# Kernel tuning notes

Measured on AMD Instinct MI355X. Metric: run time of the kernel, lower is better.

Reference implementation:

```python
import jax, jax.numpy as jnp
import numpy as np

N_NODES = 50000
N_EDGES = 800000
HID = 256
HEADS = 4
HEAD_C = HID // HEADS  # 64
IN_CH = 16
OUT_CH = 4
NEG_SLOPE = 0.2  # PyG GATConv default LeakyReLU slope
LN_EPS = 1e-5


def setup_inputs() -> dict:
    key = jax.random.key(0)
    ks = jax.random.split(key, 12)
    s = 0.05
    return {
        "x": jax.random.normal(ks[0], (N_NODES, IN_CH), dtype=jnp.float32),
        "edge_index": jax.random.randint(ks[1], (2, N_EDGES), 0, N_NODES, dtype=jnp.int64),
        "w_in": jax.random.normal(ks[2], (IN_CH, HID), dtype=jnp.float32) * s,
        "b_in": jnp.zeros((HID,), dtype=jnp.float32),
        "w_gat": jax.random.normal(ks[3], (4, HID, HID), dtype=jnp.float32) * s,
        "att_src": jax.random.normal(ks[4], (4, HEADS, HEAD_C), dtype=jnp.float32) * s,
        "att_dst": jax.random.normal(ks[5], (4, HEADS, HEAD_C), dtype=jnp.float32) * s,
        "b_gat": jnp.zeros((4, HID), dtype=jnp.float32),
        "ln_scale": jnp.ones((4, HID), dtype=jnp.float32),
        "ln_bias": jnp.zeros((4, HID), dtype=jnp.float32),
        "w_out": jax.random.normal(ks[6], (HID, OUT_CH), dtype=jnp.float32) * s,
        "b_out": jnp.zeros((OUT_CH,), dtype=jnp.float32),
    }


def _gat_layer(x, src, dst, W, a_src, a_dst, bias, g, beta):
    """One GATConv(concat, heads=4) + LayerNorm + ELU. x:[N,HID]."""
    n = x.shape[0]
    h = (x @ W).reshape(n, HEADS, HEAD_C)                 # [N,H,C]
    a_s = jnp.einsum("nhc,hc->nh", h, a_src)              # [N,H]
    a_d = jnp.einsum("nhc,hc->nh", h, a_dst)              # [N,H]
    logits = jax.nn.leaky_relu(a_s[src] + a_d[dst], NEG_SLOPE)  # [E,H]
    # segment softmax over destination neighborhoods (self-loops ensure non-empty)
    m = jax.ops.segment_max(logits, dst, num_segments=n)
    e = jnp.exp(logits - m[dst])
    denom = jax.ops.segment_sum(e, dst, num_segments=n)
    alpha = e / (denom[dst] + 1e-16)                      # [E,H]
    msg = alpha[:, :, None] * h[src]                      # [E,H,C]
    out = jax.ops.segment_sum(msg, dst, num_segments=n).reshape(n, HID) + bias
    mu = out.mean(-1, keepdims=True)
    var = out.var(-1, keepdims=True)
    out = (out - mu) * jax.lax.rsqrt(var + LN_EPS) * g + beta
    return jax.nn.elu(out)


def reference(x, edge_index, w_in, b_in, w_gat, att_src, att_dst, b_gat,
              ln_scale, ln_bias, w_out, b_out):
    n = x.shape[0]
    # PyG GATConv adds self-loops by default
    loops = jnp.arange(n, dtype=edge_index.dtype)
    ei = jnp.concatenate([edge_index, jnp.stack([loops, loops])], axis=1)
    src, dst = ei[0], ei[1]

    x = x @ w_in + b_in                                   # input_proj
    h = x
    for l in (0, 1):
        h = _gat_layer(h, src, dst, w_gat[l], att_src[l], att_dst[l],
                       b_gat[l], ln_scale[l], ln_bias[l])
    x = x + h
    h = x
    for l in (2, 3):
        h = _gat_layer(h, src, dst, w_gat[l], att_src[l], att_dst[l],
                       b_gat[l], ln_scale[l], ln_bias[l])
    x = x + h
    return x @ w_out + b_out
```

## Files before the change

kernel.cpp:

```cpp
#include <hip/hip_runtime.h>
#include <math.h>

#define NN 50000
#define E0 800000
#define ET 850000
#define HID 256
#define INCH 16
#define MAXDEG 64

#define NB_P1   416
#define EPB     2048
#define NBUCK   196

#define NB_WT   256
#define NB_IP   6250
#define NB_PREP (NB_P1 + NB_WT + NB_IP)

#define NB_G    784
#define NB_G0   (NBUCK + NB_G)

typedef _Float16 h8 __attribute__((ext_vector_type(8)));
typedef _Float16 h4 __attribute__((ext_vector_type(4)));
typedef float f32x4 __attribute__((ext_vector_type(4)));

__device__ __forceinline__ void load_lds16(const void* g, void* l) {
    __builtin_amdgcn_global_load_lds(
        (const __attribute__((address_space(1))) unsigned int*)g,
        (__attribute__((address_space(3))) unsigned int*)l, 16, 0, 0);
}

__global__ __launch_bounds__(256) void prep_kernel(
    const float* __restrict__ w_gat, _Float16* __restrict__ WT,
    const float* __restrict__ x, const float* __restrict__ w_in,
    const float* __restrict__ b_in, _Float16* __restrict__ Ph,
    const int* __restrict__ ei, unsigned int* __restrict__ pairs,
    int* __restrict__ cnt_g, int* __restrict__ off_g) {
    __shared__ unsigned int hist[256], pref[256], cur2[256];
    int b = blockIdx.x, t = threadIdx.x;
    if (b < NB_P1) {
        hist[t] = 0;
        __syncthreads();
        unsigned int pk[8];
        int base = b * EPB + t;
#pragma unroll
        for (int k = 0; k < 8; ++k) {
            int e = base + k * 256;
            pk[k] = 0xFFFFFFFFu;
            if (e < ET) {
                int s, d;
                if (e < E0) { s = ei[e]; d = ei[E0 + e]; }
                else        { s = d = e - E0; }
                pk[k] = ((unsigned int)d << 16) | (unsigned int)s;
                atomicAdd(&hist[d >> 8], 1u);
            }
        }
        __syncthreads();
        unsigned int h = hist[t];
        pref[t] = h;
        __syncthreads();
#pragma unroll
        for (int o = 1; o < 256; o <<= 1) {
            unsigned int v = (t >= o) ? pref[t - o] : 0u;
            __syncthreads();
            pref[t] += v;
            __syncthreads();
        }
        unsigned int ex = pref[t] - h;
        cur2[t] = ex;
        if (t < NBUCK) {
            cnt_g[b * NBUCK + t] = (int)h;
            off_g[b * NBUCK + t] = (int)ex;
        }
        __syncthreads();
#pragma unroll
        for (int k = 0; k < 8; ++k) {
            if (pk[k] != 0xFFFFFFFFu) {
                unsigned int g = pk[k] >> 24;
                unsigned int pos = atomicAdd(&cur2[g], 1u);
                pairs[b * EPB + pos] = pk[k];
            }
        }
    } else if (b < NB_P1 + NB_WT) {
        int k = b - NB_P1;
#pragma unroll
        for (int l = 0; l < 4; ++l) {
            float v = w_gat[((size_t)l * 256 + k) * 256 + t];
            WT[((size_t)l * 256 + t) * 256 + k] = (_Float16)v;
        }
    } else {
        int ipb = b - NB_P1 - NB_WT;
        int sub = t >> 5, l32 = t & 31;
        int n = ipb * 8 + sub;
        int c0 = l32 * 8;
        const float* xr = x + n * INCH;
        float a[8];
#pragma unroll
        for (int k = 0; k < 8; k += 4) {
            float4 bb = *(const float4*)(b_in + c0 + k);
            a[k] = bb.x; a[k + 1] = bb.y; a[k + 2] = bb.z; a[k + 3] = bb.w;
        }
#pragma unroll
        for (int k = 0; k < INCH; ++k) {
            float xv = xr[k];
            const float4 w0 = *(const float4*)(w_in + k * 256 + c0);
            const float4 w1 = *(const float4*)(w_in + k * 256 + c0 + 4);
            a[0] += xv * w0.x; a[1] += xv * w0.y; a[2] += xv * w0.z; a[3] += xv * w0.w;
            a[4] += xv * w1.x; a[5] += xv * w1.y; a[6] += xv * w1.z; a[7] += xv * w1.w;
        }
        h8 o;
#pragma unroll
        for (int k = 0; k < 8; ++k) o[k] = (_Float16)a[k];
        *(h8*)(Ph + (size_t)n * 256 + c0) = o;
    }
}

__device__ __forceinline__ void gemm_tile(
    int rb, int cb,
    const _Float16* __restrict__ A, const _Float16* __restrict__ BT,
    _Float16* __restrict__ H, const float* __restrict__ att_s,
    const float* __restrict__ att_d, float* __restrict__ AS, float* __restrict__ AD,
    _Float16* As, _Float16* Bs) {
    int t = threadIdx.x;
    int wv = t >> 6, lane = t & 63;
    int wr = (wv >> 1) * 64, wc = (wv & 1) * 64;
    int lm = lane & 15, lq = lane >> 4;
    f32x4 acc[4][4] = {};

    int rch = lane >> 2;
    int q = lane & 3;

    auto stage = [&](int k0, int buf) {
#pragma unroll
        for (int c = 0; c < 2; ++c) {
            int r = wv * 32 + c * 16 + rch;
            int g = q ^ (r & 3);
            int ra = rb + r; if (ra >= NN) ra = NN - 1;
            load_lds16(A + (size_t)ra * 256 + k0 + g * 8,
                       (char*)As + buf * 8192 + wv * 2048 + c * 1024);
            load_lds16(BT + (size_t)(cb + r) * 256 + k0 + g * 8,
                       (char*)Bs + buf * 8192 + wv * 2048 + c * 1024);
        }
    };

    stage(0, 0);
    __syncthreads();
    int cur = 0;
    for (int k0 = 0; k0 < 256; k0 += 32) {
        if (k0 + 32 < 256) stage(k0 + 32, cur ^ 1);
        h8 af[4], bfr[4];
#pragma unroll
        for (int i = 0; i < 4; ++i) {
            int row = wr + i * 16 + lm;
            af[i] = *(const h8*)((const char*)As + cur * 8192 + row * 64 + ((lq ^ (row & 3)) * 16));
        }
#pragma unroll
        for (int j = 0; j < 4; ++j) {
            int row = wc + j * 16 + lm;
            bfr[j] = *(const h8*)((const char*)Bs + cur * 8192 + row * 64 + ((lq ^ (row & 3)) * 16));
        }
#pragma unroll
        for (int i = 0; i < 4; ++i)
#pragma unroll
            for (int j = 0; j < 4; ++j)
                acc[i][j] = __builtin_amdgcn_mfma_f32_16x16x32_f16(af[i], bfr[j], acc[i][j], 0, 0, 0);
        __syncthreads();
        cur ^= 1;
    }

    int head = (cb + wc) >> 6;
    float sa[4], sd[4];
#pragma unroll
    for (int j = 0; j < 4; ++j) {
        sa[j] = att_s[head * 64 + j * 16 + lm];
        sd[j] = att_d[head * 64 + j * 16 + lm];
    }
#pragma unroll
    for (int i = 0; i < 4; ++i)
#pragma unroll
        for (int rr = 0; rr < 4; ++rr) {
            float vs = acc[i][0][rr] * sa[0] + acc[i][1][rr] * sa[1]
                     + acc[i][2][rr] * sa[2] + acc[i][3][rr] * sa[3];
            float vd = acc[i][0][rr] * sd[0] + acc[i][1][rr] * sd[1]
                     + acc[i][2][rr] * sd[2] + acc[i][3][rr] * sd[3];
#pragma unroll
            for (int o = 1; o <= 8; o <<= 1) {
                vs += __shfl_xor(vs, o, 64);
                vd += __shfl_xor(vd, o, 64);
            }
            int row = rb + wr + i * 16 + lq * 4 + rr;
            if (lm == 0 && row < NN) {
                AS[row * 4 + head] = vs;
                AD[row * 4 + head] = vd;
            }
        }

#pragma unroll
    for (int i = 0; i < 4; ++i)
#pragma unroll
        for (int j = 0; j < 4; ++j) {
            int col = cb + wc + j * 16 + lm;
#pragma unroll
            for (int rr = 0; rr < 4; ++rr) {
                int row = rb + wr + i * 16 + lq * 4 + rr;
                if (row < NN) H[(size_t)row * 256 + col] = (_Float16)acc[i][j][rr];
            }
        }
}

__device__ __forceinline__ bool gemm_map(int b, int& rb, int& cb) {
    int r = (b >> 4) * 8 + (b & 7);
    int h = (b >> 3) & 1;
    if (r >= 391) return false;
    rb = r * 128; cb = h * 128;
    return true;
}

__global__ __launch_bounds__(256) void gemm_fused_kernel(
    const _Float16* __restrict__ A, const _Float16* __restrict__ BT,
    _Float16* __restrict__ H, const float* __restrict__ att_s,
    const float* __restrict__ att_d, float* __restrict__ AS, float* __restrict__ AD) {
    __shared__ _Float16 As[2 * 128 * 32];
    __shared__ _Float16 Bs[2 * 128 * 32];
    int rb, cb;
    if (!gemm_map(blockIdx.x, rb, cb)) return;
    gemm_tile(rb, cb, A, BT, H, att_s, att_d, AS, AD, As, Bs);
}

__global__ __launch_bounds__(256) void gemm0_p2_kernel(
    const _Float16* __restrict__ A, const _Float16* __restrict__ BT,
    _Float16* __restrict__ H, const float* __restrict__ att_s,
    const float* __restrict__ att_d, float* __restrict__ AS, float* __restrict__ AD,
    const unsigned int* __restrict__ pairs, const int* __restrict__ cnt_g,
    const int* __restrict__ off_g, int* __restrict__ cursor,
    unsigned short* __restrict__ csr_pad) {
    __shared__ _Float16 As[2 * 128 * 32];
    __shared__ _Float16 Bs[2 * 128 * 32];
    int b = blockIdx.x;
    if (b < NBUCK) {
        int g = b, t = threadIdx.x;
        unsigned int* curs = (unsigned int*)As;
        curs[t] = 0;
        __syncthreads();
        for (int sb = t; sb < NB_P1; sb += 256) {
            int c = cnt_g[sb * NBUCK + g];
            int o = off_g[sb * NBUCK + g];
            const unsigned int* p = pairs + sb * EPB + o;
            for (int i = 0; i < c; ++i) {
                unsigned int pk = p[i];
                int d = (int)(pk >> 16);
                unsigned int pos = atomicAdd(&curs[d & 255], 1u);
                if (pos < MAXDEG)
                    csr_pad[((size_t)d << 6) + pos] = (unsigned short)(pk & 0xFFFFu);
            }
        }
        __syncthreads();
        int n = (g << 8) + t;
        if (n < NN) cursor[n] = (int)curs[t];
        return;
    }
    int rb, cb;
    if (!gemm_map(b - NBUCK, rb, cb)) return;
    gemm_tile(rb, cb, A, BT, H, att_s, att_d, AS, AD, As, Bs);
}

__global__ __launch_bounds__(256) void agg_kernel(
    const _Float16* __restrict__ H, const float4* __restrict__ AS,
    const float4* __restrict__ AD,
    const int* __restrict__ cnt, const unsigned short* __restrict__ csr_pad,
    const float* __restrict__ bias, const float* __restrict__ g, const float* __restrict__ beta,
    const _Float16* __restrict__ res, _Float16* __restrict__ outh,
    const float* __restrict__ wout, const float* __restrict__ bout,
    float* __restrict__ out) {
    __shared__ float eLs[4][256];
    __shared__ int   sLs[4][64];
    int t = threadIdx.x;
    int wv = t >> 6, lane = t & 63;
    int n = blockIdx.x * 4 + wv;
    int head = lane >> 4;
    int c0 = lane * 4;
    float* eL = eLs[wv];
    int*   sL = sLs[wv];

    int deg = cnt[n];
    if (deg > MAXDEG) deg = MAXDEG;
    float4 adv = AD[n];

    float4 e4 = make_float4(0.f, 0.f, 0.f, 0.f);
    int sv = 0;
    if (lane < deg) {
        sv = csr_pad[(n << 6) + lane];
        float4 as = AS[sv];
        float v0 = as.x + adv.x; v0 = (v0 >= 0.f) ? v0 : 0.2f * v0;
        float v1 = as.y + adv.y; v1 = (v1 >= 0.f) ? v1 : 0.2f * v1;
        float v2 = as.z + adv.z; v2 = (v2 >= 0.f) ? v2 : 0.2f * v2;
        float v3 = as.w + adv.w; v3 = (v3 >= 0.f) ? v3 : 0.2f * v3;
        e4 = make_float4(__expf(v0), __expf(v1), __expf(v2), __expf(v3));
    }
    sL[lane] = sv;
    *(float4*)(eL + c0) = e4;

    float acc0 = 0.f, acc1 = 0.f, acc2 = 0.f, acc3 = 0.f, acc_e = 0.f;
#pragma unroll 8
    for (int i = 0; i < deg; ++i) {
        float e = eL[i * 4 + head];
        int s = sL[i];
        h4 hv = *(const h4*)(H + (size_t)s * 256 + c0);
        acc_e += e;
        acc0 += e * (float)hv[0];
        acc1 += e * (float)hv[1];
        acc2 += e * (float)hv[2];
        acc3 += e * (float)hv[3];
    }
    float dinv = 1.f / (acc_e + 1e-16f);

    float4 bb = *(const float4*)(bias + c0);
    float val0 = acc0 * dinv + bb.x;
    float val1 = acc1 * dinv + bb.y;
    float val2 = acc2 * dinv + bb.z;
    float val3 = acc3 * dinv + bb.w;

    float s1 = val0 + val1 + val2 + val3;
    float s2 = val0 * val0 + val1 * val1 + val2 * val2 + val3 * val3;
#pragma unroll
    for (int o = 32; o >= 1; o >>= 1) {
        s1 += __shfl_xor(s1, o, 64);
        s2 += __shfl_xor(s2, o, 64);
    }
    float mu = s1 * (1.f / 256.f);
    float var = s2 * (1.f / 256.f) - mu * mu;
    float rs = rsqrtf(var + 1e-5f);

    float4 g4 = *(const float4*)(g + c0);
    float4 b4 = *(const float4*)(beta + c0);
    float y0 = (val0 - mu) * rs * g4.x + b4.x;
    float y1 = (val1 - mu) * rs * g4.y + b4.y;
    float y2 = (val2 - mu) * rs * g4.z + b4.z;
    float y3 = (val3 - mu) * rs * g4.w + b4.w;
    y0 = (y0 > 0.f) ? y0 : (__expf(y0) - 1.f);
    y1 = (y1 > 0.f) ? y1 : (__expf(y1) - 1.f);
    y2 = (y2 > 0.f) ? y2 : (__expf(y2) - 1.f);
    y3 = (y3 > 0.f) ? y3 : (__expf(y3) - 1.f);
    if (res) {
        h4 r0 = *(const h4*)(res + (size_t)n * 256 + c0);
        y0 += (float)r0[0]; y1 += (float)r0[1]; y2 += (float)r0[2]; y3 += (float)r0[3];
    }
    if (wout) {
        float4 w0 = *(const float4*)(wout + (size_t)(c0 + 0) * 4);
        float4 w1 = *(const float4*)(wout + (size_t)(c0 + 1) * 4);
        float4 w2 = *(const float4*)(wout + (size_t)(c0 + 2) * 4);
        float4 w3 = *(const float4*)(wout + (size_t)(c0 + 3) * 4);
        float o0 = y0 * w0.x + y1 * w1.x + y2 * w2.x + y3 * w3.x;
        float o1 = y0 * w0.y + y1 * w1.y + y2 * w2.y + y3 * w3.y;
        float o2 = y0 * w0.z + y1 * w1.z + y2 * w2.z + y3 * w3.z;
        float o3 = y0 * w0.w + y1 * w1.w + y2 * w2.w + y3 * w3.w;
#pragma unroll
        for (int o = 32; o >= 1; o >>= 1) {
            o0 += __shfl_xor(o0, o, 64);
            o1 += __shfl_xor(o1, o, 64);
            o2 += __shfl_xor(o2, o, 64);
            o3 += __shfl_xor(o3, o, 64);
        }
        if (lane == 0) {
            float4 ov = make_float4(o0 + bout[0], o1 + bout[1], o2 + bout[2], o3 + bout[3]);
            *(float4*)(out + (size_t)n * 4) = ov;
        }
    } else {
        h4 o0;
        o0[0] = (_Float16)y0; o0[1] = (_Float16)y1;
        o0[2] = (_Float16)y2; o0[3] = (_Float16)y3;
        *(h4*)(outh + (size_t)n * 256 + c0) = o0;
    }
}

extern "C" void kernel_launch(void* const* d_in, const int* in_sizes, int n_in,
                              void* d_out, int out_size, void* d_ws, size_t ws_size,
                              hipStream_t stream) {
    const float* x       = (const float*)d_in[0];
    const int*   ei      = (const int*)  d_in[1];
    const float* w_in    = (const float*)d_in[2];
    const float* b_in    = (const float*)d_in[3];
    const float* w_gat   = (const float*)d_in[4];
    const float* att_src = (const float*)d_in[5];
    const float* att_dst = (const float*)d_in[6];
    const float* b_gat   = (const float*)d_in[7];
    const float* ln_g    = (const float*)d_in[8];
    const float* ln_b    = (const float*)d_in[9];
    const float* w_out   = (const float*)d_in[10];
    const float* b_out   = (const float*)d_in[11];
    float* out = (float*)d_out;

    char* ws = (char*)d_ws;
    size_t off = 0;
    auto alloc = [&](size_t bytes) {
        void* p = ws + off;
        off += (bytes + 255) & ~(size_t)255;
        return p;
    };
    _Float16*       Ph      = (_Float16*)alloc((size_t)NN * HID * 2);
    _Float16*       Ch      = (_Float16*)alloc((size_t)NN * HID * 2);
    _Float16*       Gh      = (_Float16*)alloc((size_t)NN * HID * 2);
    _Float16*       H       = (_Float16*)alloc((size_t)NN * HID * 2);
    _Float16*       WT      = (_Float16*)alloc((size_t)4 * HID * HID * 2);
    float*          ASAD    = (float*)alloc((size_t)NN * 8 * 4);
    int*            cursor  = (int*)alloc((size_t)NN * 4);
    unsigned short* csr_pad = (unsigned short*)alloc((size_t)NN * MAXDEG * 2);
    unsigned int*   pairs   = (unsigned int*)alloc((size_t)NB_P1 * EPB * 4);
    int*            cnt_g   = (int*)alloc((size_t)NB_P1 * NBUCK * 4);
    int*            off_g   = (int*)alloc((size_t)NB_P1 * NBUCK * 4);

    float* AS = ASAD;
    float* AD = ASAD + (size_t)NN * 4;

    const int NB_AGG = NN / 4;

    prep_kernel<<<NB_PREP, 256, 0, stream>>>(w_gat, WT, x, w_in, b_in, Ph,
                                             ei, pairs, cnt_g, off_g);

    gemm0_p2_kernel<<<NB_G0, 256, 0, stream>>>(
        Ph, WT, H, att_src, att_dst, AS, AD, pairs, cnt_g, off_g, cursor, csr_pad);
    agg_kernel<<<NB_AGG, 256, 0, stream>>>(
        H, (const float4*)AS, (const float4*)AD, cursor, csr_pad,
        b_gat, ln_g, ln_b, nullptr, Gh, nullptr, nullptr, nullptr);

    auto run_layer = [&](const _Float16* inh, int l, const _Float16* res, _Float16* outh,
                         const float* wo, const float* bo) {
        gemm_fused_kernel<<<NB_G, 256, 0, stream>>>(
            inh, WT + (size_t)l * HID * HID, H,
            att_src + l * 256, att_dst + l * 256, AS, AD);
        agg_kernel<<<NB_AGG, 256, 0, stream>>>(
            H, (const float4*)AS, (const float4*)AD, cursor, csr_pad,
            b_gat + l * 256, ln_g + l * 256, ln_b + l * 256, res, outh, wo, bo,
            wo ? out : nullptr);
    };

    run_layer(Gh, 1, Ph,      Ch, nullptr, nullptr);
    run_layer(Ch, 2, nullptr, Gh, nullptr, nullptr);
    run_layer(Gh, 3, Ch,      Ph, w_out,   b_out);
}
```

Measured before the change: 506.5 us.

## Split aggregation into per-slice gather kernels with slice-major H and separate LayerNorm

The GEMM now writes H in a slice-major layout of 8 column slices of 32 halves per node. A new slice aggregation kernel gathers neighbours one slice at a time, with block index mod 8 picking the slice. The intent is that each XCD gathers from a ~3.2MB slice that can stay resident in its L2, instead of scattering 512B row reads over the full 25.6MB H. Softmax normalisation moves into the slice kernel, and LayerNorm, ELU, residual and output projection move to a separate kernel that reads an fp16 intermediate. This adds an extra round trip to global memory and an extra launch per layer.

```diff
diff --git a/kernel.cpp b/kernel.cpp
--- a/kernel.cpp
+++ b/kernel.cpp
@@ -18,6 +18,11 @@
 
 #define NB_G    784
 #define NB_G0   (NBUCK + NB_G)
+
+#define NPW_S   8
+#define NB_SL   (8 * ((NN + 4 * NPW_S - 1) / (4 * NPW_S)))
+#define NPW_L   4
+#define NB_LN   (NN / (4 * NPW_L))
 
 typedef _Float16 h8 __attribute__((ext_vector_type(8)));
 typedef _Float16 h4 __attribute__((ext_vector_type(4)));
@@ -199,10 +204,11 @@
 #pragma unroll
         for (int j = 0; j < 4; ++j) {
             int col = cb + wc + j * 16 + lm;
+            _Float16* Hc = H + (size_t)(col >> 5) * NN * 32 + (col & 31);
 #pragma unroll
             for (int rr = 0; rr < 4; ++rr) {
                 int row = rb + wr + i * 16 + lq * 4 + rr;
-                if (row < NN) H[(size_t)row * 256 + col] = (_Float16)acc[i][j][rr];
+                if (row < NN) Hc[(size_t)row * 32] = (_Float16)acc[i][j][rr];
             }
         }
 }
@@ -263,112 +269,142 @@
     gemm_tile(rb, cb, A, BT, H, att_s, att_d, AS, AD, As, Bs);
 }
 
-__global__ __launch_bounds__(256) void agg_kernel(
-    const _Float16* __restrict__ H, const float4* __restrict__ AS,
-    const float4* __restrict__ AD,
+__global__ __launch_bounds__(256) void slice_agg_kernel(
+    const _Float16* __restrict__ H,
+    const float* __restrict__ AS,
+    const float* __restrict__ AD,
     const int* __restrict__ cnt, const unsigned short* __restrict__ csr_pad,
+    _Float16* __restrict__ tmp) {
+    __shared__ float alS[4][80];
+    __shared__ int   slS[4][80];
+    int t = threadIdx.x;
+    int wv = t >> 6, lane = t & 63;
+    int b = blockIdx.x;
+    int s = b & 7;
+    int h = s >> 1;
+    int grp = b >> 3;
+    const _Float16* Hs = H + (size_t)s * NN * 32;
+    float* al = alS[wv];
+    int*   sl = slS[wv];
+    int eg = lane >> 3;
+    int cc = (lane & 7) * 4;
+
+    for (int k = 0; k < NPW_S; ++k) {
+        int n = (grp * 4 + wv) * NPW_S + k;
+        if (n >= NN) break;
+        int deg = cnt[n];
+        if (deg > MAXDEG) deg = MAXDEG;
+        float e_i = 0.f;
+        int sv = 0;
+        if (lane < deg) {
+            sv = csr_pad[(n << 6) + lane];
+            float v = AS[sv * 4 + h] + AD[n * 4 + h];
+            v = (v >= 0.f) ? v : 0.2f * v;
+            e_i = __expf(v);
+        }
+        float den = e_i;
+#pragma unroll
+        for (int o = 1; o <= 32; o <<= 1) den += __shfl_xor(den, o, 64);
+        float alpha = e_i / den;
+        al[lane] = alpha;
+        sl[lane] = sv;
+        if (lane < 16) { al[64 + lane] = 0.f; sl[64 + lane] = 0; }
+        float a0 = 0.f, a1 = 0.f, a2 = 0.f, a3 = 0.f;
+        for (int i = 0; i < deg; i += 8) {
+            int e = i + eg;
+            float a = al[e];
+            int src = sl[e];
+            h4 hv = *(const h4*)(Hs + (size_t)src * 32 + cc);
+            a0 += a * (float)hv[0];
+            a1 += a * (float)hv[1];
+            a2 += a * (float)hv[2];
+            a3 += a * (float)hv[3];
+        }
+#pragma unroll
+        for (int o = 8; o <= 32; o <<= 1) {
+            a0 += __shfl_xor(a0, o, 64);
+            a1 += __shfl_xor(a1, o, 64);
+            a2 += __shfl_xor(a2, o, 64);
+            a3 += __shfl_xor(a3, o, 64);
+        }
+        if (lane < 8) {
+            h4 ov;
+            ov[0] = (_Float16)a0; ov[1] = (_Float16)a1;
+            ov[2] = (_Float16)a2; ov[3] = (_Float16)a3;
+            *(h4*)(tmp + (size_t)n * 256 + s * 32 + lane * 4) = ov;
+        }
+    }
+}
+
+__global__ __launch_bounds__(256) void ln_kernel(
+    const _Float16* __restrict__ tmp,
     const float* __restrict__ bias, const float* __restrict__ g, const float* __restrict__ beta,
     const _Float16* __restrict__ res, _Float16* __restrict__ outh,
     const float* __restrict__ wout, const float* __restrict__ bout,
     float* __restrict__ out) {
-    __shared__ float eLs[4][256];
-    __shared__ int   sLs[4][64];
     int t = threadIdx.x;
     int wv = t >> 6, lane = t & 63;
-    int n = blockIdx.x * 4 + wv;
-    int head = lane >> 4;
     int c0 = lane * 4;
-    float* eL = eLs[wv];
-    int*   sL = sLs[wv];
-
-    int deg = cnt[n];
-    if (deg > MAXDEG) deg = MAXDEG;
-    float4 adv = AD[n];
-
-    float4 e4 = make_float4(0.f, 0.f, 0.f, 0.f);
-    int sv = 0;
-    if (lane < deg) {
-        sv = csr_pad[(n << 6) + lane];
-        float4 as = AS[sv];
-        float v0 = as.x + adv.x; v0 = (v0 >= 0.f) ? v0 : 0.2f * v0;
-        float v1 = as.y + adv.y; v1 = (v1 >= 0.f) ? v1 : 0.2f * v1;
-        float v2 = as.z + adv.z; v2 = (v2 >= 0.f) ? v2 : 0.2f * v2;
-        float v3 = as.w + adv.w; v3 = (v3 >= 0.f) ? v3 : 0.2f * v3;
-        e4 = make_float4(__expf(v0), __expf(v1), __expf(v2), __expf(v3));
-    }
-    sL[lane] = sv;
-    *(float4*)(eL + c0) = e4;
-
-    float acc0 = 0.f, acc1 = 0.f, acc2 = 0.f, acc3 = 0.f, acc_e = 0.f;
-#pragma unroll 8
-    for (int i = 0; i < deg; ++i) {
-        float e = eL[i * 4 + head];
-        int s = sL[i];
-        h4 hv = *(const h4*)(H + (size_t)s * 256 + c0);
-        acc_e += e;
-        acc0 += e * (float)hv[0];
-        acc1 += e * (float)hv[1];
-        acc2 += e * (float)hv[2];
-        acc3 += e * (float)hv[3];
-    }
-    float dinv = 1.f / (acc_e + 1e-16f);
-
     float4 bb = *(const float4*)(bias + c0);
-    float val0 = acc0 * dinv + bb.x;
-    float val1 = acc1 * dinv + bb.y;
-    float val2 = acc2 * dinv + bb.z;
-    float val3 = acc3 * dinv + bb.w;
-
-    float s1 = val0 + val1 + val2 + val3;
-    float s2 = val0 * val0 + val1 * val1 + val2 * val2 + val3 * val3;
-#pragma unroll
-    for (int o = 32; o >= 1; o >>= 1) {
-        s1 += __shfl_xor(s1, o, 64);
-        s2 += __shfl_xor(s2, o, 64);
-    }
-    float mu = s1 * (1.f / 256.f);
-    float var = s2 * (1.f / 256.f) - mu * mu;
-    float rs = rsqrtf(var + 1e-5f);
-
     float4 g4 = *(const float4*)(g + c0);
     float4 b4 = *(const float4*)(beta + c0);
-    float y0 = (val0 - mu) * rs * g4.x + b4.x;
-    float y1 = (val1 - mu) * rs * g4.y + b4.y;
-    float y2 = (val2 - mu) * rs * g4.z + b4.z;
-    float y3 = (val3 - mu) * rs * g4.w + b4.w;
-    y0 = (y0 > 0.f) ? y0 : (__expf(y0) - 1.f);
-    y1 = (y1 > 0.f) ? y1 : (__expf(y1) - 1.f);
-    y2 = (y2 > 0.f) ? y2 : (__expf(y2) - 1.f);
-    y3 = (y3 > 0.f) ? y3 : (__expf(y3) - 1.f);
-    if (res) {
-        h4 r0 = *(const h4*)(res + (size_t)n * 256 + c0);
-        y0 += (float)r0[0]; y1 += (float)r0[1]; y2 += (float)r0[2]; y3 += (float)r0[3];
-    }
-    if (wout) {
-        float4 w0 = *(const float4*)(wout + (size_t)(c0 + 0) * 4);
-        float4 w1 = *(const float4*)(wout + (size_t)(c0 + 1) * 4);
-        float4 w2 = *(const float4*)(wout + (size_t)(c0 + 2) * 4);
-        float4 w3 = *(const float4*)(wout + (size_t)(c0 + 3) * 4);
-        float o0 = y0 * w0.x + y1 * w1.x + y2 * w2.x + y3 * w3.x;
-        float o1 = y0 * w0.y + y1 * w1.y + y2 * w2.y + y3 * w3.y;
-        float o2 = y0 * w0.z + y1 * w1.z + y2 * w2.z + y3 * w3.z;
-        float o3 = y0 * w0.w + y1 * w1.w + y2 * w2.w + y3 * w3.w;
+    for (int k = 0; k < NPW_L; ++k) {
+        int n = (blockIdx.x * 4 + wv) * NPW_L + k;
+        h4 v = *(const h4*)(tmp + (size_t)n * 256 + c0);
+        float val0 = (float)v[0] + bb.x;
+        float val1 = (float)v[1] + bb.y;
+        float val2 = (float)v[2] + bb.z;
+        float val3 = (float)v[3] + bb.w;
+
+        float s1 = val0 + val1 + val2 + val3;
+        float s2 = val0 * val0 + val1 * val1 + val2 * val2 + val3 * val3;
 #pragma unroll
         for (int o = 32; o >= 1; o >>= 1) {
-            o0 += __shfl_xor(o0, o, 64);
-            o1 += __shfl_xor(o1, o, 64);
-            o2 += __shfl_xor(o2, o, 64);
-            o3 += __shfl_xor(o3, o, 64);
-        }
-        if (lane == 0) {
-            float4 ov = make_float4(o0 + bout[0], o1 + bout[1], o2 + bout[2], o3 + bout[3]);
-            *(float4*)(out + (size_t)n * 4) = ov;
-        }
-    } else {
-        h4 o0;
-        o0[0] = (_Float16)y0; o0[1] = (_Float16)y1;
-        o0[2] = (_Float16)y2; o0[3] = (_Float16)y3;
-        *(h4*)(outh + (size_t)n * 256 + c0) = o0;
+            s1 += __shfl_xor(s1, o, 64);
+            s2 += __shfl_xor(s2, o, 64);
+        }
+        float mu = s1 * (1.f / 256.f);
+        float var = s2 * (1.f / 256.f) - mu * mu;
+        float rs = rsqrtf(var + 1e-5f);
+
+        float y0 = (val0 - mu) * rs * g4.x + b4.x;
+        float y1 = (val1 - mu) * rs * g4.y + b4.y;
+        float y2 = (val2 - mu) * rs * g4.z + b4.z;
+        float y3 = (val3 - mu) * rs * g4.w + b4.w;
+        y0 = (y0 > 0.f) ? y0 : (__expf(y0) - 1.f);
+        y1 = (y1 > 0.f) ? y1 : (__expf(y1) - 1.f);
+        y2 = (y2 > 0.f) ? y2 : (__expf(y2) - 1.f);
+        y3 = (y3 > 0.f) ? y3 : (__expf(y3) - 1.f);
+        if (res) {
+            h4 r0 = *(const h4*)(res + (size_t)n * 256 + c0);
+            y0 += (float)r0[0]; y1 += (float)r0[1]; y2 += (float)r0[2]; y3 += (float)r0[3];
+        }
+        if (wout) {
+            float4 w0 = *(const float4*)(wout + (size_t)(c0 + 0) * 4);
+            float4 w1 = *(const float4*)(wout + (size_t)(c0 + 1) * 4);
+            float4 w2 = *(const float4*)(wout + (size_t)(c0 + 2) * 4);
+            float4 w3 = *(const float4*)(wout + (size_t)(c0 + 3) * 4);
+            float o0 = y0 * w0.x + y1 * w1.x + y2 * w2.x + y3 * w3.x;
+            float o1 = y0 * w0.y + y1 * w1.y + y2 * w2.y + y3 * w3.y;
+            float o2 = y0 * w0.z + y1 * w1.z + y2 * w2.z + y3 * w3.z;
+            float o3 = y0 * w0.w + y1 * w1.w + y2 * w2.w + y3 * w3.w;
+#pragma unroll
+            for (int o = 32; o >= 1; o >>= 1) {
+                o0 += __shfl_xor(o0, o, 64);
+                o1 += __shfl_xor(o1, o, 64);
+                o2 += __shfl_xor(o2, o, 64);
+                o3 += __shfl_xor(o3, o, 64);
+            }
+            if (lane == 0) {
+                float4 ov = make_float4(o0 + bout[0], o1 + bout[1], o2 + bout[2], o3 + bout[3]);
+                *(float4*)(out + (size_t)n * 4) = ov;
+            }
+        } else {
+            h4 o0;
+            o0[0] = (_Float16)y0; o0[1] = (_Float16)y1;
+            o0[2] = (_Float16)y2; o0[3] = (_Float16)y3;
+            *(h4*)(outh + (size_t)n * 256 + c0) = o0;
+        }
     }
 }
 
@@ -411,29 +447,27 @@
     float* AS = ASAD;
     float* AD = ASAD + (size_t)NN * 4;
 
-    const int NB_AGG = NN / 4;
-
     prep_kernel<<<NB_PREP, 256, 0, stream>>>(w_gat, WT, x, w_in, b_in, Ph,
                                              ei, pairs, cnt_g, off_g);
 
     gemm0_p2_kernel<<<NB_G0, 256, 0, stream>>>(
         Ph, WT, H, att_src, att_dst, AS, AD, pairs, cnt_g, off_g, cursor, csr_pad);
-    agg_kernel<<<NB_AGG, 256, 0, stream>>>(
-        H, (const float4*)AS, (const float4*)AD, cursor, csr_pad,
-        b_gat, ln_g, ln_b, nullptr, Gh, nullptr, nullptr, nullptr);
+    slice_agg_kernel<<<NB_SL, 256, 0, stream>>>(H, AS, AD, cursor, csr_pad, Ch);
+    ln_kernel<<<NB_LN, 256, 0, stream>>>(Ch, b_gat, ln_g, ln_b,
+                                         nullptr, Gh, nullptr, nullptr, nullptr);
 
     auto run_layer = [&](const _Float16* inh, int l, const _Float16* res, _Float16* outh,
-                         const float* wo, const float* bo) {
+                         _Float16* tmp, const float* wo, const float* bo) {
         gemm_fused_kernel<<<NB_G, 256, 0, stream>>>(
             inh, WT + (size_t)l * HID * HID, H,
             att_src + l * 256, att_dst + l * 256, AS, AD);
-        agg_kernel<<<NB_AGG, 256, 0, stream>>>(
-            H, (const float4*)AS, (const float4*)AD, cursor, csr_pad,
-            b_gat + l * 256, ln_g + l * 256, ln_b + l * 256, res, outh, wo, bo,
-            wo ? out : nullptr);
+        slice_agg_kernel<<<NB_SL, 256, 0, stream>>>(H, AS, AD, cursor, csr_pad, tmp);
+        ln_kernel<<<NB_LN, 256, 0, stream>>>(tmp, b_gat + l * 256, ln_g + l * 256,
+                                             ln_b + l * 256, res, outh, wo, bo,
+                                             wo ? out : nullptr);
     };
 
-    run_layer(Gh, 1, Ph,      Ch, nullptr, nullptr);
-    run_layer(Ch, 2, nullptr, Gh, nullptr, nullptr);
-    run_layer(Gh, 3, Ch,      Ph, w_out,   b_out);
-}
+    run_layer(Gh, 1, Ph,      Ch, Gh, nullptr, nullptr);
+    run_layer(Ch, 2, nullptr, Gh, Ph, nullptr, nullptr);
+    run_layer(Gh, 3, Ch,      Ph, Gh, w_out,   b_out);
+}
```

After: 829.3 us. +63.7%, slower.

## Load full B tile into LDS once and stream A fragments from global

Applied to the files above, without the earlier changes.

The GEMM tile now stages the whole 128x256 weight slice into LDS up front (64KB) instead of double-buffering both A and B per K step. A fragments are read directly from global memory into registers, with a one-step register prefetch, which removes the per-iteration __syncthreads. The agg loop unroll also drops from 8 to 4. The larger LDS footprint limits how many blocks fit per CU, and A reads from global are uncoalesced row fragments.

```diff
diff --git a/kernel.cpp b/kernel.cpp
--- a/kernel.cpp
+++ b/kernel.cpp
@@ -119,7 +119,7 @@
     const _Float16* __restrict__ A, const _Float16* __restrict__ BT,
     _Float16* __restrict__ H, const float* __restrict__ att_s,
     const float* __restrict__ att_d, float* __restrict__ AS, float* __restrict__ AD,
-    _Float16* As, _Float16* Bs) {
+    _Float16* Bs) {
     int t = threadIdx.x;
     int wv = t >> 6, lane = t & 63;
     int wr = (wv >> 1) * 64, wc = (wv & 1) * 64;
@@ -129,42 +129,51 @@
     int rch = lane >> 2;
     int q = lane & 3;
 
-    auto stage = [&](int k0, int buf) {
+#pragma unroll
+    for (int c8 = 0; c8 < 8; ++c8) {
+        int k0 = c8 * 32;
 #pragma unroll
         for (int c = 0; c < 2; ++c) {
             int r = wv * 32 + c * 16 + rch;
             int g = q ^ (r & 3);
-            int ra = rb + r; if (ra >= NN) ra = NN - 1;
-            load_lds16(A + (size_t)ra * 256 + k0 + g * 8,
-                       (char*)As + buf * 8192 + wv * 2048 + c * 1024);
             load_lds16(BT + (size_t)(cb + r) * 256 + k0 + g * 8,
-                       (char*)Bs + buf * 8192 + wv * 2048 + c * 1024);
-        }
-    };
-
-    stage(0, 0);
+                       (char*)Bs + c8 * 8192 + wv * 2048 + c * 1024);
+        }
+    }
+
+    const _Float16* arow[4];
+#pragma unroll
+    for (int i = 0; i < 4; ++i) {
+        int ra = rb + wr + i * 16 + lm;
+        if (ra >= NN) ra = NN - 1;
+        arow[i] = A + (size_t)ra * 256 + lq * 8;
+    }
+
+    h8 afc[4], afn[4];
+#pragma unroll
+    for (int i = 0; i < 4; ++i) afc[i] = *(const h8*)(arow[i]);
+
     __syncthreads();
-    int cur = 0;
-    for (int k0 = 0; k0 < 256; k0 += 32) {
-        if (k0 + 32 < 256) stage(k0 + 32, cur ^ 1);
-        h8 af[4], bfr[4];
-#pragma unroll
-        for (int i = 0; i < 4; ++i) {
-            int row = wr + i * 16 + lm;
-            af[i] = *(const h8*)((const char*)As + cur * 8192 + row * 64 + ((lq ^ (row & 3)) * 16));
-        }
+
+#pragma unroll
+    for (int c8 = 0; c8 < 8; ++c8) {
+        if (c8 < 7) {
+#pragma unroll
+            for (int i = 0; i < 4; ++i) afn[i] = *(const h8*)(arow[i] + (c8 + 1) * 32);
+        }
+        h8 bfr[4];
 #pragma unroll
         for (int j = 0; j < 4; ++j) {
             int row = wc + j * 16 + lm;
-            bfr[j] = *(const h8*)((const char*)Bs + cur * 8192 + row * 64 + ((lq ^ (row & 3)) * 16));
+            bfr[j] = *(const h8*)((const char*)Bs + c8 * 8192 + row * 64 + ((lq ^ (row & 3)) * 16));
         }
 #pragma unroll
         for (int i = 0; i < 4; ++i)
 #pragma unroll
             for (int j = 0; j < 4; ++j)
-                acc[i][j] = __builtin_amdgcn_mfma_f32_16x16x32_f16(af[i], bfr[j], acc[i][j], 0, 0, 0);
-        __syncthreads();
-        cur ^= 1;
+                acc[i][j] = __builtin_amdgcn_mfma_f32_16x16x32_f16(afc[i], bfr[j], acc[i][j], 0, 0, 0);
+#pragma unroll
+        for (int i = 0; i < 4; ++i) afc[i] = afn[i];
     }
 
     int head = (cb + wc) >> 6;
@@ -219,11 +228,10 @@
     const _Float16* __restrict__ A, const _Float16* __restrict__ BT,
     _Float16* __restrict__ H, const float* __restrict__ att_s,
     const float* __restrict__ att_d, float* __restrict__ AS, float* __restrict__ AD) {
-    __shared__ _Float16 As[2 * 128 * 32];
-    __shared__ _Float16 Bs[2 * 128 * 32];
+    __shared__ _Float16 Bs[8 * 4096];
     int rb, cb;
     if (!gemm_map(blockIdx.x, rb, cb)) return;
-    gemm_tile(rb, cb, A, BT, H, att_s, att_d, AS, AD, As, Bs);
+    gemm_tile(rb, cb, A, BT, H, att_s, att_d, AS, AD, Bs);
 }
 
 __global__ __launch_bounds__(256) void gemm0_p2_kernel(
@@ -233,12 +241,11 @@
     const unsigned int* __restrict__ pairs, const int* __restrict__ cnt_g,
     const int* __restrict__ off_g, int* __restrict__ cursor,
     unsigned short* __restrict__ csr_pad) {
-    __shared__ _Float16 As[2 * 128 * 32];
-    __shared__ _Float16 Bs[2 * 128 * 32];
+    __shared__ _Float16 Bs[8 * 4096];
     int b = blockIdx.x;
     if (b < NBUCK) {
         int g = b, t = threadIdx.x;
-        unsigned int* curs = (unsigned int*)As;
+        unsigned int* curs = (unsigned int*)Bs;
         curs[t] = 0;
         __syncthreads();
         for (int sb = t; sb < NB_P1; sb += 256) {
@@ -260,7 +267,7 @@
     }
     int rb, cb;
     if (!gemm_map(b - NBUCK, rb, cb)) return;
-    gemm_tile(rb, cb, A, BT, H, att_s, att_d, AS, AD, As, Bs);
+    gemm_tile(rb, cb, A, BT, H, att_s, att_d, AS, AD, Bs);
 }
 
 __global__ __launch_bounds__(256) void agg_kernel(
@@ -300,7 +307,7 @@
     *(float4*)(eL + c0) = e4;
 
     float acc0 = 0.f, acc1 = 0.f, acc2 = 0.f, acc3 = 0.f, acc_e = 0.f;
-#pragma unroll 8
+#pragma unroll 4
     for (int i = 0; i < deg; ++i) {
         float e = eL[i * 4 + head];
         int s = sL[i];
```

Measured after the change: 525.4 us. 1.04x slower.
